# Kernel optimization log

Hardware: AMD Instinct MI355X
Metric: run time of the kernel (lower is better)

Reference implementation:

```python
import jax, jax.numpy as jnp
import numpy as np

KH, KW = 3, 3
SH, SW = 1, 1
IC, OC = 32, 32
M = 4
P = M * M
ITERS = 3
LAM = 1.0
EPS = 1e-8


def _patches(t, kh, kw, sh, sw):
    # t: [B, H, W, ...] -> [B, Ho, Wo, kh, kw, ...] (im2col, matches torch unfold+permute)
    H, W = t.shape[1], t.shape[2]
    Ho = (H - kh) // sh + 1
    Wo = (W - kw) // sw + 1
    i = (jnp.arange(Ho) * sh)[:, None] + jnp.arange(kh)[None, :]  # [Ho,kh]
    j = (jnp.arange(Wo) * sw)[:, None] + jnp.arange(kw)[None, :]  # [Wo,kw]
    tp = t[:, i]            # [B,Ho,kh,W,...]
    tp = tp[:, :, :, j]     # [B,Ho,kh,Wo,kw,...]
    return jnp.moveaxis(tp, 2, 3)  # [B,Ho,Wo,kh,kw,...]


def setup_inputs() -> dict:
    key = jax.random.key(0)
    k1, k2, k3, k4, k5 = jax.random.split(key, 5)
    x = jax.random.normal(k1, (4, 14, 14, IC, M, M), dtype=jnp.float32)
    a = jax.random.uniform(k2, (4, 14, 14, IC), dtype=jnp.float32)
    W = jax.random.uniform(k3, (KH, KW, IC, OC, M, M), dtype=jnp.float32)   # torch.rand init
    beta_u = jax.random.uniform(k4, (1, OC, 1), dtype=jnp.float32)
    beta_a = jax.random.uniform(k5, (1, OC), dtype=jnp.float32)
    return {"x": x, "a": a, "W": W, "beta_u": beta_u, "beta_a": beta_a}


def reference(x, a, W, beta_u, beta_a):
    # im2col patches
    xp = _patches(x, KH, KW, SH, SW)          # [B,Ho,Wo,kh,kw,IC,M,M]
    ap = _patches(a, KH, KW, SH, SW)          # [B,Ho,Wo,kh,kw,IC]
    # pose-transform votes: per (kh,kw,inCap,outCap) 4x4 matmul
    V = jnp.einsum('bhwklcxy,klcoyz->bhwklcoxz', xp, W)
    B, Ho, Wo = V.shape[:3]
    N = KH * KW * IC
    V = V.reshape(B, Ho, Wo, N, OC, P)        # votes
    a_in = ap.reshape(B, Ho, Wo, N)
    bu = beta_u.reshape(OC, 1)
    ba = beta_a.reshape(OC)

    # EM routing (Hinton et al. 2018, fixed inverse temperature)
    R = jnp.full((B, Ho, Wo, N, OC), 1.0 / OC, dtype=V.dtype)
    for it in range(ITERS):
        Ra = R * a_in[..., None]                                  # [B,Ho,Wo,N,OC]
        Rs = Ra.sum(axis=3) + EPS                                 # [B,Ho,Wo,OC]
        mu = jnp.einsum('bhwno,bhwnop->bhwop', Ra, V) / Rs[..., None]
        d = V - mu[:, :, :, None]                                 # [B,Ho,Wo,N,OC,P]
        sig2 = jnp.einsum('bhwno,bhwnop->bhwop', Ra, d * d) / Rs[..., None] + EPS
        cost = (bu + 0.5 * jnp.log(sig2)) * Rs[..., None]         # [B,Ho,Wo,OC,P]
        a_out = jax.nn.sigmoid(LAM * (ba - cost.sum(-1)))         # [B,Ho,Wo,OC]
        if it < ITERS - 1:
            logp = -0.5 * jnp.sum(d * d / sig2[:, :, :, None] + jnp.log(sig2)[:, :, :, None], axis=-1)
            R = jax.nn.softmax(jnp.log(a_out + EPS)[:, :, :, None] + logp, axis=-1)

    pose = mu.reshape(B, Ho, Wo, OC, M, M)
    return pose, a_out
```

## Files before the change

### kernel.cpp

```cpp
#include <hip/hip_runtime.h>


#define NN    288
#define EPSV  1e-8f

__device__ __forceinline__ void compute_votes(const float* __restrict__ Wt,
                                              const float* __restrict__ xp_s,
                                              int n, int o, float* __restrict__ V)
{
  float Wf[16];
  {
    const float* wp = Wt + (((n << 5) + o) << 4);
#pragma unroll
    for (int i = 0; i < 4; ++i) {
      const float4 q = *(const float4*)(wp + (i << 2));
      Wf[i*4+0]=q.x; Wf[i*4+1]=q.y; Wf[i*4+2]=q.z; Wf[i*4+3]=q.w;
    }
  }
  float xv[16];
  {
    const float* xr = xp_s + (n << 4);
#pragma unroll
    for (int i = 0; i < 4; ++i) {
      const float4 q = *(const float4*)(xr + (i << 2));
      xv[i*4+0]=q.x; xv[i*4+1]=q.y; xv[i*4+2]=q.z; xv[i*4+3]=q.w;
    }
  }
#pragma unroll
  for (int xi = 0; xi < 4; ++xi)
#pragma unroll
    for (int z = 0; z < 4; ++z)
      V[xi*4+z] = fmaf(xv[xi*4+0], Wf[z],
                  fmaf(xv[xi*4+1], Wf[4+z],
                  fmaf(xv[xi*4+2], Wf[8+z],
                       xv[xi*4+3]* Wf[12+z])));
}

__global__ __launch_bounds__(512, 4) void caps_em_kernel(
    const float* __restrict__ X, const float* __restrict__ A, const float* __restrict__ Wt,
    const float* __restrict__ Bu, const float* __restrict__ Ba,
    float* __restrict__ Out)
{
  __shared__ float xp_s[NN*16];
  __shared__ float a_s[NN];
  __shared__ float part[8*544];
  __shared__ float prs[8*32];
  __shared__ float mu_t[512];
  __shared__ float isig_t[512];
  __shared__ float lsig_t[512];
  __shared__ float la_s[32];
  __shared__ float slog_s[32];
  __shared__ float aout_s[32];

  const int t    = threadIdx.x;
  const int o    = t & 31;
  const int ng   = t >> 5;
  const int wv   = t >> 6;
  const int lane = t & 63;

  const int pos = blockIdx.x;
  const int b  = pos / 144;
  const int r_ = pos - b*144;
  const int h  = r_ / 12;
  const int w  = r_ - (r_/12)*12;

  for (int i = t; i < 1152; i += 512) {
    const int e   = i << 2;
    const int kl  = e >> 9;
    const int rem = e & 511;
    const int hy = h + kl/3, wx = w + (kl - (kl/3)*3);
    const float4 q = *(const float4*)(X + ((((b*14 + hy)*14 + wx) << 9) + rem));
    *(float4*)(xp_s + (kl << 9) + rem) = q;
  }
  for (int i = t; i < NN; i += 512) {
    const int kl = i >> 5, c = i & 31;
    const int hy = h + kl/3, wx = w + (kl - (kl/3)*3);
    a_s[i] = A[((b*14 + hy)*14 + wx)*32 + c];
  }
  __syncthreads();

  float mu_r[16], isig_r[16];
  float la_r = 0.f, slog_r = 0.f;
#pragma unroll
  for (int p = 0; p < 16; ++p) { mu_r[p] = 0.f; isig_r[p] = 0.f; }

  for (int it = 0; it < 3; ++it) {
    float S1[16], S2[16];
#pragma unroll
    for (int p = 0; p < 16; ++p) { S1[p] = 0.f; S2[p] = 0.f; }
    float rs = 0.f;

#pragma unroll 1
    for (int j = 0; j < 18; ++j) {
      const int n = ng + (j << 4);
      float V[16];
      compute_votes(Wt, xp_s, n, o, V);

      float ra;
      if (it == 0) {
        ra = a_s[n] * (1.0f/32.0f);
      } else {
        float q = slog_r;
#pragma unroll
        for (int p = 0; p < 16; ++p) {
          const float d = V[p] - mu_r[p];
          q = fmaf(d*d, isig_r[p], q);
        }
        float z = la_r - 0.5f*q;
        float m = z;
#pragma unroll
        for (int msk = 16; msk >= 1; msk >>= 1) m = fmaxf(m, __shfl_xor(m, msk));
        float ev = __expf(z - m);
        float s = ev;
#pragma unroll
        for (int msk = 16; msk >= 1; msk >>= 1) s += __shfl_xor(s, msk);
        ra = (ev / s) * a_s[n];
      }
      rs += ra;
#pragma unroll
      for (int p = 0; p < 16; ++p) {
        const float rv = ra * V[p];
        S1[p] += rv;
        S2[p] = fmaf(rv, V[p], S2[p]);
      }
    }

#pragma unroll
    for (int p = 0; p < 16; ++p) {
      S1[p] += __shfl_xor(S1[p], 32);
      S2[p] += __shfl_xor(S2[p], 32);
    }
    rs += __shfl_xor(rs, 32);

    if (lane < 32) {
      float* p1 = part + wv*544 + o*17;
#pragma unroll
      for (int p = 0; p < 16; ++p) p1[p] = S1[p];
      prs[wv*32 + o] = rs;
    }
    __syncthreads();
    {
      const int pi = t >> 5, oo = t & 31;
      float s1 = 0.f, rsum = EPSV;
#pragma unroll
      for (int g = 0; g < 8; ++g) {
        s1   += part[g*544 + oo*17 + pi];
        rsum += prs[(g << 5) + oo];
      }
      mu_t[pi*32 + oo] = s1 / rsum;
    }
    __syncthreads();

    if (lane < 32) {
      float* p2 = part + wv*544 + o*17;
#pragma unroll
      for (int p = 0; p < 16; ++p) p2[p] = S2[p];
    }
    __syncthreads();
    {
      const int pi = t >> 5, oo = t & 31;
      float s2 = 0.f, rsum = EPSV;
#pragma unroll
      for (int g = 0; g < 8; ++g) {
        s2   += part[g*544 + oo*17 + pi];
        rsum += prs[(g << 5) + oo];
      }
      const float mu = mu_t[pi*32 + oo];
      float var = s2 / rsum - mu*mu;
      var = fmaxf(var, 0.f);
      const float sg = var + EPSV;
      isig_t[pi*32 + oo] = 1.0f / sg;
      lsig_t[pi*32 + oo] = __logf(sg);
    }
    __syncthreads();

    if (t < 32) {
      float rsum = EPSV;
#pragma unroll
      for (int g = 0; g < 8; ++g) rsum += prs[(g << 5) + t];
      float slog = 0.f;
#pragma unroll
      for (int p = 0; p < 16; ++p) slog += lsig_t[p*32 + t];
      const float bu = Bu[t];
      const float ba = Ba[t];
      const float cost = rsum * (16.0f*bu + 0.5f*slog);
      const float av = 1.0f / (1.0f + __expf(-(ba - cost)));
      aout_s[t] = av;
      la_s[t]   = __logf(av + EPSV);
      slog_s[t] = slog;
    }
    __syncthreads();

    if (it < 2) {
#pragma unroll
      for (int p = 0; p < 16; ++p) {
        mu_r[p]   = mu_t[p*32 + o];
        isig_r[p] = isig_t[p*32 + o];
      }
      slog_r = slog_s[o];
      la_r   = la_s[o];
    }
  }

  {
    const int oo = t >> 4, pi = t & 15;
    Out[pos*512 + t] = mu_t[pi*32 + oo];
  }
  if (t < 32) Out[294912 + pos*32 + t] = aout_s[t];
}

extern "C" void kernel_launch(void* const* d_in, const int* in_sizes, int n_in,
                              void* d_out, int out_size, void* d_ws, size_t ws_size,
                              hipStream_t stream) {
  (void)in_sizes; (void)n_in; (void)d_ws; (void)ws_size; (void)out_size;
  const float* X  = (const float*)d_in[0];
  const float* A  = (const float*)d_in[1];
  const float* Wt = (const float*)d_in[2];
  const float* Bu = (const float*)d_in[3];
  const float* Ba = (const float*)d_in[4];
  float* Out = (float*)d_out;
  hipLaunchKernelGGL(caps_em_kernel, dim3(576), dim3(512), 0, stream,
                     X, A, Wt, Bu, Ba, Out);
}
```

Before: 177.4 us.

## Software-pipeline W loads across vote iterations and read mu/isig from LDS

The vote loop is unrolled by two, and the weight matrices for the next capsule are prefetched from global memory into registers while the current votes are computed. This is meant to hide global load latency. The per-thread mu and 1/sigma register arrays are dropped. Those values are now read as packed float2 pairs from shared memory inside the loop, which frees registers for the prefetch buffers but adds LDS traffic in each iteration.

```diff
diff --git a/kernel.cpp b/kernel.cpp
--- a/kernel.cpp
+++ b/kernel.cpp
@@ -4,36 +4,19 @@
 #define NN    288
 #define EPSV  1e-8f
 
-__device__ __forceinline__ void compute_votes(const float* __restrict__ Wt,
-                                              const float* __restrict__ xp_s,
-                                              int n, int o, float* __restrict__ V)
+__device__ __forceinline__ void votes_from(const float4 w0, const float4 w1,
+                                           const float4 w2, const float4 w3,
+                                           const float* __restrict__ xr,
+                                           float* __restrict__ V)
 {
-  float Wf[16];
-  {
-    const float* wp = Wt + (((n << 5) + o) << 4);
-#pragma unroll
-    for (int i = 0; i < 4; ++i) {
-      const float4 q = *(const float4*)(wp + (i << 2));
-      Wf[i*4+0]=q.x; Wf[i*4+1]=q.y; Wf[i*4+2]=q.z; Wf[i*4+3]=q.w;
-    }
-  }
-  float xv[16];
-  {
-    const float* xr = xp_s + (n << 4);
-#pragma unroll
-    for (int i = 0; i < 4; ++i) {
-      const float4 q = *(const float4*)(xr + (i << 2));
-      xv[i*4+0]=q.x; xv[i*4+1]=q.y; xv[i*4+2]=q.z; xv[i*4+3]=q.w;
-    }
-  }
-#pragma unroll
-  for (int xi = 0; xi < 4; ++xi)
-#pragma unroll
-    for (int z = 0; z < 4; ++z)
-      V[xi*4+z] = fmaf(xv[xi*4+0], Wf[z],
-                  fmaf(xv[xi*4+1], Wf[4+z],
-                  fmaf(xv[xi*4+2], Wf[8+z],
-                       xv[xi*4+3]* Wf[12+z])));
+#pragma unroll
+  for (int x = 0; x < 4; ++x) {
+    const float4 xq = *(const float4*)(xr + (x << 2));
+    V[x*4+0] = fmaf(xq.x, w0.x, fmaf(xq.y, w1.x, fmaf(xq.z, w2.x, xq.w*w3.x)));
+    V[x*4+1] = fmaf(xq.x, w0.y, fmaf(xq.y, w1.y, fmaf(xq.z, w2.y, xq.w*w3.y)));
+    V[x*4+2] = fmaf(xq.x, w0.z, fmaf(xq.y, w1.z, fmaf(xq.z, w2.z, xq.w*w3.z)));
+    V[x*4+3] = fmaf(xq.x, w0.w, fmaf(xq.y, w1.w, fmaf(xq.z, w2.w, xq.w*w3.w)));
+  }
 }
 
 __global__ __launch_bounds__(512, 4) void caps_em_kernel(
@@ -41,16 +24,16 @@
     const float* __restrict__ Bu, const float* __restrict__ Ba,
     float* __restrict__ Out)
 {
-  __shared__ float xp_s[NN*16];
-  __shared__ float a_s[NN];
-  __shared__ float part[8*544];
-  __shared__ float prs[8*32];
-  __shared__ float mu_t[512];
-  __shared__ float isig_t[512];
-  __shared__ float lsig_t[512];
-  __shared__ float la_s[32];
-  __shared__ float slog_s[32];
-  __shared__ float aout_s[32];
+  __shared__ float  xp_s[NN*16];
+  __shared__ float  a_s[NN];
+  __shared__ float  part[8*544];
+  __shared__ float  prs[8*32];
+  __shared__ float  mu_t[512];
+  __shared__ float2 misg_t[512];
+  __shared__ float  lsig_t[512];
+  __shared__ float  la_s[32];
+  __shared__ float  slog_s[32];
+  __shared__ float  aout_s[32];
 
   const int t    = threadIdx.x;
   const int o    = t & 31;
@@ -79,10 +62,7 @@
   }
   __syncthreads();
 
-  float mu_r[16], isig_r[16];
   float la_r = 0.f, slog_r = 0.f;
-#pragma unroll
-  for (int p = 0; p < 16; ++p) { mu_r[p] = 0.f; isig_r[p] = 0.f; }
 
   for (int it = 0; it < 3; ++it) {
     float S1[16], S2[16];
@@ -90,38 +70,70 @@
     for (int p = 0; p < 16; ++p) { S1[p] = 0.f; S2[p] = 0.f; }
     float rs = 0.f;
 
+    float4 bA0, bA1, bA2, bA3, bB0, bB1, bB2, bB3;
+    {
+      const float* wp = Wt + (((ng << 5) + o) << 4);
+      bA0 = *(const float4*)(wp);
+      bA1 = *(const float4*)(wp + 4);
+      bA2 = *(const float4*)(wp + 8);
+      bA3 = *(const float4*)(wp + 12);
+    }
+
 #pragma unroll 1
-    for (int j = 0; j < 18; ++j) {
-      const int n = ng + (j << 4);
-      float V[16];
-      compute_votes(Wt, xp_s, n, o, V);
-
-      float ra;
-      if (it == 0) {
-        ra = a_s[n] * (1.0f/32.0f);
-      } else {
-        float q = slog_r;
+    for (int jj = 0; jj < 9; ++jj) {
+      const int nA = ng + (jj << 5);
+      const int nB = nA + 16;
+      {
+        const float* wp = Wt + (((nB << 5) + o) << 4);
+        bB0 = *(const float4*)(wp);
+        bB1 = *(const float4*)(wp + 4);
+        bB2 = *(const float4*)(wp + 8);
+        bB3 = *(const float4*)(wp + 12);
+      }
+
+#pragma unroll
+      for (int half = 0; half < 2; ++half) {
+        const int n = half ? nB : nA;
+        float V[16];
+        if (half) votes_from(bB0, bB1, bB2, bB3, xp_s + (n << 4), V);
+        else      votes_from(bA0, bA1, bA2, bA3, xp_s + (n << 4), V);
+
+        if (!half && jj < 8) {
+          const float* wp = Wt + ((((nA + 32) << 5) + o) << 4);
+          bA0 = *(const float4*)(wp);
+          bA1 = *(const float4*)(wp + 4);
+          bA2 = *(const float4*)(wp + 8);
+          bA3 = *(const float4*)(wp + 12);
+        }
+
+        float ra;
+        if (it == 0) {
+          ra = a_s[n] * (1.0f/32.0f);
+        } else {
+          float q = slog_r;
+#pragma unroll
+          for (int p = 0; p < 16; ++p) {
+            const float2 ms = misg_t[p*32 + o];
+            const float d = V[p] - ms.x;
+            q = fmaf(d*d, ms.y, q);
+          }
+          float z = la_r - 0.5f*q;
+          float m = z;
+#pragma unroll
+          for (int msk = 16; msk >= 1; msk >>= 1) m = fmaxf(m, __shfl_xor(m, msk));
+          const float ev = __expf(z - m);
+          float s = ev;
+#pragma unroll
+          for (int msk = 16; msk >= 1; msk >>= 1) s += __shfl_xor(s, msk);
+          ra = (ev / s) * a_s[n];
+        }
+        rs += ra;
 #pragma unroll
         for (int p = 0; p < 16; ++p) {
-          const float d = V[p] - mu_r[p];
-          q = fmaf(d*d, isig_r[p], q);
+          const float rv = ra * V[p];
+          S1[p] += rv;
+          S2[p] = fmaf(rv, V[p], S2[p]);
         }
-        float z = la_r - 0.5f*q;
-        float m = z;
-#pragma unroll
-        for (int msk = 16; msk >= 1; msk >>= 1) m = fmaxf(m, __shfl_xor(m, msk));
-        float ev = __expf(z - m);
-        float s = ev;
-#pragma unroll
-        for (int msk = 16; msk >= 1; msk >>= 1) s += __shfl_xor(s, msk);
-        ra = (ev / s) * a_s[n];
-      }
-      rs += ra;
-#pragma unroll
-      for (int p = 0; p < 16; ++p) {
-        const float rv = ra * V[p];
-        S1[p] += rv;
-        S2[p] = fmaf(rv, V[p], S2[p]);
       }
     }
 
@@ -169,7 +181,7 @@
       float var = s2 / rsum - mu*mu;
       var = fmaxf(var, 0.f);
       const float sg = var + EPSV;
-      isig_t[pi*32 + oo] = 1.0f / sg;
+      misg_t[pi*32 + oo] = make_float2(mu, 1.0f / sg);
       lsig_t[pi*32 + oo] = __logf(sg);
     }
     __syncthreads();
@@ -192,11 +204,6 @@
     __syncthreads();
 
     if (it < 2) {
-#pragma unroll
-      for (int p = 0; p < 16; ++p) {
-        mu_r[p]   = mu_t[p*32 + o];
-        isig_r[p] = isig_t[p*32 + o];
-      }
       slog_r = slog_s[o];
       la_r   = la_s[o];
     }
```

Result: slower. 199.8 us (+12.6%).
